# Kernel optimization log

Measured on AMD Instinct MI355X. Metric: run time of the kernel, lower is better.

## Reference

```python
import math
import jax, jax.numpy as jnp
import numpy as np

D_MODEL = 1024
N_HEADS = 16
D_HEAD = D_MODEL // N_HEADS


def get_alibi_slopes(n_heads: int) -> np.ndarray:
    def pow2_slopes(n):
        start = 2 ** (-2 ** (-(math.log2(n) - 3)))
        return np.array([start * start ** i for i in range(n)], dtype=np.float32)
    if math.log2(n_heads).is_integer():
        return pow2_slopes(n_heads)
    closest = 2 ** math.floor(math.log2(n_heads))
    slopes = pow2_slopes(closest)
    extra = pow2_slopes(2 * closest)[0::2][: n_heads - closest]
    return np.concatenate([slopes, extra], axis=0)


def setup_inputs() -> dict:
    key = jax.random.key(0)
    ks = jax.random.split(key, 9)
    B, S, D = 2, 2048, D_MODEL
    scale = 1.0 / math.sqrt(D)
    inp = {
        "x": jax.random.normal(ks[0], (B, S, D), dtype=jnp.float32),
        "Wq": jax.random.normal(ks[1], (D, D), dtype=jnp.float32) * scale,
        "bq": jnp.zeros((D,), dtype=jnp.float32),
        "Wk": jax.random.normal(ks[2], (D, D), dtype=jnp.float32) * scale,
        "bk": jnp.zeros((D,), dtype=jnp.float32),
        "Wv": jax.random.normal(ks[3], (D, D), dtype=jnp.float32) * scale,
        "bv": jnp.zeros((D,), dtype=jnp.float32),
        "Wo": jax.random.normal(ks[4], (D, D), dtype=jnp.float32) * scale,
        "bo": jnp.zeros((D,), dtype=jnp.float32),
    }
    return inp


def reference(x, Wq, bq, Wk, bk, Wv, bv, Wo, bo):
    B, S, D = x.shape
    H, Dh = N_HEADS, D_HEAD
    # projections (torch Linear: x @ W.T + b)
    q = (x @ Wq.T + bq).reshape(B, S, H, Dh).transpose(0, 2, 1, 3)  # [B,H,S,Dh]
    k = (x @ Wk.T + bk).reshape(B, S, H, Dh).transpose(0, 2, 1, 3)
    v = (x @ Wv.T + bv).reshape(B, S, H, Dh).transpose(0, 2, 1, 3)

    scores = jnp.einsum("bhqd,bhkd->bhqk", q, k) / math.sqrt(Dh)  # [B,H,S,S]

    slopes = jnp.asarray(get_alibi_slopes(H), dtype=scores.dtype)  # [H]
    pos = jnp.arange(S, dtype=scores.dtype)
    pos_diff = pos[None, :] - pos[:, None]                         # [S,S] (k - q)
    alibi = slopes[:, None, None] * pos_diff[None, :, :]           # [H,S,S]
    scores = scores + alibi[None]

    causal = jnp.tril(jnp.ones((S, S), dtype=bool))
    scores = jnp.where(causal[None, None], scores, -jnp.inf)

    weights = jax.nn.softmax(scores, axis=-1)
    y = jnp.einsum("bhqk,bhkd->bhqd", weights, v)                  # [B,H,S,Dh]
    y = y.transpose(0, 2, 1, 3).reshape(B, S, D)
    return y @ Wo.T + bo
```

## Files before the change

### kernel.cpp

```cpp
#include <hip/hip_runtime.h>

typedef unsigned short u16;
typedef unsigned int u32;
typedef short bf16x8 __attribute__((ext_vector_type(8)));
typedef float f32x4 __attribute__((ext_vector_type(4)));
typedef u16 u16x4 __attribute__((ext_vector_type(4)));

#define D_MODEL 1024
#define NHEADS 16
#define DHEAD 64
#define BATCH 2
#define SEQ 2048
#define NROWS (BATCH * SEQ)
#define NTILES (SEQ / 64)

static __device__ __forceinline__ u16 f2bf(float f) {
  u32 x = __float_as_uint(f);
  x += 0x7fffu + ((x >> 16) & 1u);
  return (u16)(x >> 16);
}

#define GLL16(gp, lp)                                             \
  __builtin_amdgcn_global_load_lds(                               \
      (const __attribute__((address_space(1))) u32*)(gp),         \
      (__attribute__((address_space(3))) u32*)(lp), 16, 0, 0)

__global__ __launch_bounds__(256) void castk(const float* __restrict__ in,
                                             u16* __restrict__ out, int n4) {
  int i = blockIdx.x * 256 + threadIdx.x;
  if (i >= n4) return;
  float4 v = ((const float4*)in)[i];
  u32 lo = (u32)f2bf(v.x) | ((u32)f2bf(v.y) << 16);
  u32 hi = (u32)f2bf(v.z) | ((u32)f2bf(v.w) << 16);
  ((uint2*)out)[i] = make_uint2(lo, hi);
}

__global__ __launch_bounds__(256) void castw(const float* __restrict__ w0,
                                             const float* __restrict__ w1,
                                             const float* __restrict__ w2,
                                             const float* __restrict__ w3,
                                             u16* __restrict__ o0,
                                             u16* __restrict__ o1,
                                             u16* __restrict__ o2,
                                             u16* __restrict__ o3) {
  const int z = blockIdx.z;
  const float* in = (z == 0) ? w0 : (z == 1) ? w1 : (z == 2) ? w2 : w3;
  u16* out = (z == 0) ? o0 : (z == 1) ? o1 : (z == 2) ? o2 : o3;
  int i = blockIdx.x * 256 + threadIdx.x;
  float4 v = ((const float4*)in)[i];
  u32 lo = (u32)f2bf(v.x) | ((u32)f2bf(v.y) << 16);
  u32 hi = (u32)f2bf(v.z) | ((u32)f2bf(v.w) << 16);
  ((uint2*)out)[i] = make_uint2(lo, hi);
}

template <int MODE>
__device__ __forceinline__ void gemm_core(const u16* __restrict__ A,
                                          const u16* __restrict__ Bw,
                                          const float* __restrict__ bias,
                                          u16* __restrict__ ob,
                                          float* __restrict__ of,
                                          int bm, int bn) {
  constexpr int K = 1024, N = 1024;
  __shared__ __attribute__((aligned(16))) u16 As[128 * 32];
  __shared__ __attribute__((aligned(16))) u16 Bs[128 * 32];
  const int tx = threadIdx.x;
  const int w = tx >> 6, lane = tx & 63;
  const int wm = w >> 1, wn = w & 1;
  const int c = lane & 15, g = lane >> 4;
  f32x4 acc[4][4];
  for (int m = 0; m < 4; ++m)
    for (int n = 0; n < 4; ++n) acc[m][n] = {0.f, 0.f, 0.f, 0.f};
  const int srow = w * 16 + (lane >> 2);
  const int sck = (lane & 3) * 8;
  for (int k0 = 0; k0 < K; k0 += 32) {
    for (int m = 0; m < 2; ++m) {
      GLL16(A + (size_t)(bm + m * 64 + srow) * K + k0 + sck,
            (char*)As + m * 4096 + w * 1024);
      GLL16(Bw + (size_t)(bn + m * 64 + srow) * K + k0 + sck,
            (char*)Bs + m * 4096 + w * 1024);
    }
    __syncthreads();
    bf16x8 af[4], bf_[4];
    for (int m = 0; m < 4; ++m)
      af[m] = *(const bf16x8*)(As + (wm * 64 + m * 16 + c) * 32 + g * 8);
    for (int n = 0; n < 4; ++n)
      bf_[n] = *(const bf16x8*)(Bs + (wn * 64 + n * 16 + c) * 32 + g * 8);
    for (int m = 0; m < 4; ++m)
      for (int n = 0; n < 4; ++n)
        acc[m][n] = __builtin_amdgcn_mfma_f32_16x16x32_bf16(af[m], bf_[n],
                                                            acc[m][n], 0, 0, 0);
    __syncthreads();
  }
  for (int n = 0; n < 4; ++n) {
    const int col = bn + wn * 64 + n * 16 + c;
    const float bv = bias[col];
    for (int m = 0; m < 4; ++m) {
      if (MODE == 2) {
        const int rs = bm + wm * 64 + m * 16 + g * 4;
        u16x4 pk;
        for (int r = 0; r < 4; ++r) pk[r] = f2bf(acc[m][n][r] + bv);
        const size_t vrow = (size_t)((rs >> 11) * NHEADS + (col >> 6)) * DHEAD +
                            (col & 63);
        *(u16x4*)(ob + vrow * SEQ + (rs & 2047)) = pk;
      } else {
        for (int r = 0; r < 4; ++r) {
          const int row = bm + wm * 64 + m * 16 + g * 4 + r;
          float v = acc[m][n][r] + bv;
          if (MODE == 1)
            of[(size_t)row * N + col] = v;
          else
            ob[(size_t)row * N + col] = f2bf(v);
        }
      }
    }
  }
}

__global__ __launch_bounds__(256) void gemm_qkv(const u16* __restrict__ xb,
                                                const u16* __restrict__ wq,
                                                const u16* __restrict__ wk,
                                                const float* __restrict__ bq,
                                                const float* __restrict__ bk,
                                                u16* __restrict__ q,
                                                u16* __restrict__ k) {
  const int z = blockIdx.z;
  const u16* W = (z == 0) ? wq : wk;
  const float* bi = (z == 0) ? bq : bk;
  u16* o = (z == 0) ? q : k;
  gemm_core<0>(xb, W, bi, o, nullptr, blockIdx.y * 128, blockIdx.x * 128);
}

__global__ __launch_bounds__(256) void gemm_v(const u16* __restrict__ xb,
                                              const u16* __restrict__ wv,
                                              const float* __restrict__ bv,
                                              u16* __restrict__ vt) {
  gemm_core<2>(xb, wv, bv, vt, nullptr, blockIdx.y * 128, blockIdx.x * 128);
}

__global__ __launch_bounds__(256) void gemm_o(const u16* __restrict__ yb,
                                              const u16* __restrict__ wo,
                                              const float* __restrict__ bo,
                                              float* __restrict__ out) {
  gemm_core<1>(yb, wo, bo, nullptr, out, blockIdx.y * 128, blockIdx.x * 128);
}

__global__ __launch_bounds__(256) void attn(const u16* __restrict__ qb,
                                            const u16* __restrict__ kb,
                                            const u16* __restrict__ vt,
                                            u16* __restrict__ yb) {
  __shared__ __attribute__((aligned(16))) u16 Qs[64 * 64];
  __shared__ __attribute__((aligned(16))) u16 Ks[2 * 64 * 64];
  __shared__ __attribute__((aligned(16))) u16 Vs[2 * 64 * 64];
  __shared__ __attribute__((aligned(16))) u16 Ps[4 * 16 * 64];
  const int tx = threadIdx.x;
  const int w = tx >> 6, lane = tx & 63;
  const int c = lane & 15, g = lane >> 4;
  const int bh = blockIdx.y;
  const int b = bh >> 4, h = bh & 15;
  const size_t rb = (size_t)b * SEQ;
  const size_t vtb = (size_t)bh * DHEAD;
  const float slope2 = exp2f(-0.5f * (float)(h + 1)) * 1.44269504f;
  const float S2 = 0.125f * 1.44269504f;

  const int strow = w * 8 + (lane >> 3);
  const int stck = lane & 7;

  for (int pass = 0; pass < 2; ++pass) {
    const int qi = pass ? (NTILES - 1 - blockIdx.x) : blockIdx.x;
    const int q0 = qi * 64;
    if (pass) __syncthreads();

    for (int m = 0; m < 2; ++m) {
      int row = m * 32 + strow;
      GLL16(qb + (rb + q0 + row) * D_MODEL + h * DHEAD +
                ((stck ^ (row & 7)) * 8),
            (char*)Qs + m * 4096 + w * 1024);
      GLL16(kb + (rb + row) * D_MODEL + h * DHEAD + ((stck ^ (row & 7)) * 8),
            (char*)Ks + m * 4096 + w * 1024);
      GLL16(vt + (vtb + row) * SEQ + ((stck ^ (row & 7)) * 8),
            (char*)Vs + m * 4096 + w * 1024);
    }

    float mrun[4], lsum[4];
    f32x4 acc[4];
    for (int r = 0; r < 4; ++r) { mrun[r] = -1e30f; lsum[r] = 0.f; }
    for (int d = 0; d < 4; ++d) acc[d] = {0.f, 0.f, 0.f, 0.f};
    const float qrow[4] = {(float)(q0 + w * 16 + g * 4 + 0),
                           (float)(q0 + w * 16 + g * 4 + 1),
                           (float)(q0 + w * 16 + g * 4 + 2),
                           (float)(q0 + w * 16 + g * 4 + 3)};
    const int qrowi = q0 + w * 16 + g * 4;

    int cur = 0;
    for (int kt = 0; kt <= qi; ++kt) {
      __syncthreads();
      if (kt < qi) {
        for (int m = 0; m < 2; ++m) {
          int row = m * 32 + strow;
          GLL16(kb + (rb + (kt + 1) * 64 + row) * D_MODEL + h * DHEAD +
                    ((stck ^ (row & 7)) * 8),
                (char*)Ks + (cur ^ 1) * 8192 + m * 4096 + w * 1024);
          GLL16(vt + (vtb + row) * SEQ + (kt + 1) * 64 +
                    ((stck ^ (row & 7)) * 8),
                (char*)Vs + (cur ^ 1) * 8192 + m * 4096 + w * 1024);
        }
      }

      bf16x8 aq[2];
      for (int ks = 0; ks < 2; ++ks)
        aq[ks] = *(const bf16x8*)((const char*)Qs + (w * 16 + c) * 128 +
                                  ((ks * 64 + g * 16) ^ ((c & 7) << 4)));
      f32x4 sc[4];
      for (int n = 0; n < 4; ++n) {
        sc[n] = {0.f, 0.f, 0.f, 0.f};
        for (int ks = 0; ks < 2; ++ks) {
          bf16x8 bk = *(const bf16x8*)((const char*)Ks + cur * 8192 +
                                       (n * 16 + c) * 128 +
                                       ((ks * 64 + g * 16) ^ ((c & 7) << 4)));
          sc[n] =
              __builtin_amdgcn_mfma_f32_16x16x32_bf16(aq[ks], bk, sc[n], 0, 0, 0);
        }
      }

      const int kbase = kt * 64 + c;
      const bool diag = (kt == qi);
      float p[4][4];
      for (int r = 0; r < 4; ++r) {
        const float base = slope2 * ((float)kbase - qrow[r]);
        float srow_[4];
        float rmax = -1e30f;
        for (int n = 0; n < 4; ++n) {
          float s = fmaf(sc[n][r], S2, base + slope2 * (float)(n * 16));
          if (diag && (kbase + n * 16 > qrowi + r)) s = -1e30f;
          srow_[n] = s;
          rmax = fmaxf(rmax, s);
        }
        for (int off = 1; off < 16; off <<= 1)
          rmax = fmaxf(rmax, __shfl_xor(rmax, off));
        const float mn = fmaxf(mrun[r], rmax);
        const float corr = exp2f(mrun[r] - mn);
        mrun[r] = mn;
        float rsum = 0.f;
        for (int n = 0; n < 4; ++n) {
          float pv = exp2f(srow_[n] - mn);
          p[n][r] = pv;
          rsum += pv;
        }
        for (int off = 1; off < 16; off <<= 1) rsum += __shfl_xor(rsum, off);
        lsum[r] = lsum[r] * corr + rsum;
        for (int d = 0; d < 4; ++d) acc[d][r] *= corr;
      }

      for (int n = 0; n < 4; ++n)
        for (int r = 0; r < 4; ++r) {
          const int row = g * 4 + r;
          *(u16*)((char*)Ps + w * 2048 + row * 128 +
                  (((n * 16 + c) * 2) ^ ((row & 7) << 4))) = f2bf(p[n][r]);
        }

      for (int ks = 0; ks < 2; ++ks) {
        bf16x8 pa = *(const bf16x8*)((const char*)Ps + w * 2048 + c * 128 +
                                     ((ks * 64 + g * 16) ^ ((c & 7) << 4)));
        for (int d = 0; d < 4; ++d) {
          bf16x8 vb_ = *(const bf16x8*)((const char*)Vs + cur * 8192 +
                                        (d * 16 + c) * 128 +
                                        ((ks * 64 + g * 16) ^ ((c & 7) << 4)));
          acc[d] = __builtin_amdgcn_mfma_f32_16x16x32_bf16(pa, vb_, acc[d], 0, 0, 0);
        }
      }
      cur ^= 1;
    }

    for (int d = 0; d < 4; ++d)
      for (int r = 0; r < 4; ++r) {
        const int qlocal = w * 16 + g * 4 + r;
        float o = acc[d][r] / lsum[r];
        yb[(rb + q0 + qlocal) * D_MODEL + h * DHEAD + d * 16 + c] = f2bf(o);
      }
  }
}

extern "C" void kernel_launch(void* const* d_in, const int* in_sizes, int n_in,
                              void* d_out, int out_size, void* d_ws,
                              size_t ws_size, hipStream_t stream) {
  const float* x = (const float*)d_in[0];
  const float* Wq = (const float*)d_in[1];
  const float* bq = (const float*)d_in[2];
  const float* Wk = (const float*)d_in[3];
  const float* bk = (const float*)d_in[4];
  const float* Wv = (const float*)d_in[5];
  const float* bv = (const float*)d_in[6];
  const float* Wo = (const float*)d_in[7];
  const float* bo = (const float*)d_in[8];
  float* out = (float*)d_out;

  char* ws = (char*)d_ws;
  u16* xb = (u16*)(ws + (size_t)0);
  u16* wqb = (u16*)(ws + ((size_t)8 << 20));
  u16* wkb = (u16*)(ws + ((size_t)10 << 20));
  u16* wvb = (u16*)(ws + ((size_t)12 << 20));
  u16* wob = (u16*)(ws + ((size_t)14 << 20));
  u16* qb = (u16*)(ws + ((size_t)16 << 20));
  u16* kb = (u16*)(ws + ((size_t)24 << 20));
  u16* vtb = (u16*)(ws + ((size_t)32 << 20));
  u16* yb = xb;

  castk<<<4096, 256, 0, stream>>>(x, xb, NROWS * D_MODEL / 4);
  castw<<<dim3(1024, 1, 4), 256, 0, stream>>>(Wq, Wk, Wv, Wo, wqb, wkb, wvb,
                                              wob);

  gemm_qkv<<<dim3(8, 32, 2), 256, 0, stream>>>(xb, wqb, wkb, bq, bk, qb, kb);
  gemm_v<<<dim3(8, 32, 1), 256, 0, stream>>>(xb, wvb, bv, vtb);
  attn<<<dim3(NTILES / 2, 32, 1), 256, 0, stream>>>(qb, kb, vtb, yb);
  gemm_o<<<dim3(8, 32, 1), 256, 0, stream>>>(yb, wob, bo, out);
}
```

Measured before the change: 245.8 us.

## Double-buffer GEMM K-tiles, reschedule attention grid, compute row sums via MFMA

```diff
diff --git a/kernel.cpp b/kernel.cpp
--- a/kernel.cpp
+++ b/kernel.cpp
@@ -61,8 +61,8 @@
                                           float* __restrict__ of,
                                           int bm, int bn) {
   constexpr int K = 1024, N = 1024;
-  __shared__ __attribute__((aligned(16))) u16 As[128 * 32];
-  __shared__ __attribute__((aligned(16))) u16 Bs[128 * 32];
+  __shared__ __attribute__((aligned(16))) u16 As[2][128 * 32];
+  __shared__ __attribute__((aligned(16))) u16 Bs[2][128 * 32];
   const int tx = threadIdx.x;
   const int w = tx >> 6, lane = tx & 63;
   const int wm = w >> 1, wn = w & 1;
@@ -72,24 +72,33 @@
     for (int n = 0; n < 4; ++n) acc[m][n] = {0.f, 0.f, 0.f, 0.f};
   const int srow = w * 16 + (lane >> 2);
   const int sck = (lane & 3) * 8;
+  for (int m = 0; m < 2; ++m) {
+    GLL16(A + (size_t)(bm + m * 64 + srow) * K + sck,
+          (char*)As[0] + m * 4096 + w * 1024);
+    GLL16(Bw + (size_t)(bn + m * 64 + srow) * K + sck,
+          (char*)Bs[0] + m * 4096 + w * 1024);
+  }
+  int cur = 0;
   for (int k0 = 0; k0 < K; k0 += 32) {
-    for (int m = 0; m < 2; ++m) {
-      GLL16(A + (size_t)(bm + m * 64 + srow) * K + k0 + sck,
-            (char*)As + m * 4096 + w * 1024);
-      GLL16(Bw + (size_t)(bn + m * 64 + srow) * K + k0 + sck,
-            (char*)Bs + m * 4096 + w * 1024);
-    }
     __syncthreads();
+    if (k0 + 32 < K) {
+      for (int m = 0; m < 2; ++m) {
+        GLL16(A + (size_t)(bm + m * 64 + srow) * K + k0 + 32 + sck,
+              (char*)As[cur ^ 1] + m * 4096 + w * 1024);
+        GLL16(Bw + (size_t)(bn + m * 64 + srow) * K + k0 + 32 + sck,
+              (char*)Bs[cur ^ 1] + m * 4096 + w * 1024);
+      }
+    }
     bf16x8 af[4], bf_[4];
     for (int m = 0; m < 4; ++m)
-      af[m] = *(const bf16x8*)(As + (wm * 64 + m * 16 + c) * 32 + g * 8);
+      af[m] = *(const bf16x8*)(As[cur] + (wm * 64 + m * 16 + c) * 32 + g * 8);
     for (int n = 0; n < 4; ++n)
-      bf_[n] = *(const bf16x8*)(Bs + (wn * 64 + n * 16 + c) * 32 + g * 8);
+      bf_[n] = *(const bf16x8*)(Bs[cur] + (wn * 64 + n * 16 + c) * 32 + g * 8);
     for (int m = 0; m < 4; ++m)
       for (int n = 0; n < 4; ++n)
         acc[m][n] = __builtin_amdgcn_mfma_f32_16x16x32_bf16(af[m], bf_[n],
                                                             acc[m][n], 0, 0, 0);
-    __syncthreads();
+    cur ^= 1;
   }
   for (int n = 0; n < 4; ++n) {
     const int col = bn + wn * 64 + n * 16 + c;
@@ -149,14 +158,17 @@
                                             const u16* __restrict__ vt,
                                             u16* __restrict__ yb) {
   __shared__ __attribute__((aligned(16))) u16 Qs[64 * 64];
-  __shared__ __attribute__((aligned(16))) u16 Ks[2 * 64 * 64];
-  __shared__ __attribute__((aligned(16))) u16 Vs[2 * 64 * 64];
+  __shared__ __attribute__((aligned(16))) u16 Ks[2][64 * 64];
+  __shared__ __attribute__((aligned(16))) u16 Vs[2][64 * 64];
   __shared__ __attribute__((aligned(16))) u16 Ps[4 * 16 * 64];
   const int tx = threadIdx.x;
   const int w = tx >> 6, lane = tx & 63;
   const int c = lane & 15, g = lane >> 4;
-  const int bh = blockIdx.y;
+  const int f = blockIdx.x;
+  const int bh = (f & 7) * 4 + ((f >> 3) & 3);
+  const int qi = NTILES - 1 - (f >> 5);
   const int b = bh >> 4, h = bh & 15;
+  const int q0 = qi * 64;
   const size_t rb = (size_t)b * SEQ;
   const size_t vtb = (size_t)bh * DHEAD;
   const float slope2 = exp2f(-0.5f * (float)(h + 1)) * 1.44269504f;
@@ -165,119 +177,108 @@
   const int strow = w * 8 + (lane >> 3);
   const int stck = lane & 7;
 
-  for (int pass = 0; pass < 2; ++pass) {
-    const int qi = pass ? (NTILES - 1 - blockIdx.x) : blockIdx.x;
-    const int q0 = qi * 64;
-    if (pass) __syncthreads();
-
-    for (int m = 0; m < 2; ++m) {
-      int row = m * 32 + strow;
-      GLL16(qb + (rb + q0 + row) * D_MODEL + h * DHEAD +
-                ((stck ^ (row & 7)) * 8),
-            (char*)Qs + m * 4096 + w * 1024);
-      GLL16(kb + (rb + row) * D_MODEL + h * DHEAD + ((stck ^ (row & 7)) * 8),
-            (char*)Ks + m * 4096 + w * 1024);
-      GLL16(vt + (vtb + row) * SEQ + ((stck ^ (row & 7)) * 8),
-            (char*)Vs + m * 4096 + w * 1024);
-    }
-
-    float mrun[4], lsum[4];
-    f32x4 acc[4];
-    for (int r = 0; r < 4; ++r) { mrun[r] = -1e30f; lsum[r] = 0.f; }
-    for (int d = 0; d < 4; ++d) acc[d] = {0.f, 0.f, 0.f, 0.f};
-    const float qrow[4] = {(float)(q0 + w * 16 + g * 4 + 0),
-                           (float)(q0 + w * 16 + g * 4 + 1),
-                           (float)(q0 + w * 16 + g * 4 + 2),
-                           (float)(q0 + w * 16 + g * 4 + 3)};
-    const int qrowi = q0 + w * 16 + g * 4;
-
-    int cur = 0;
-    for (int kt = 0; kt <= qi; ++kt) {
-      __syncthreads();
-      if (kt < qi) {
-        for (int m = 0; m < 2; ++m) {
-          int row = m * 32 + strow;
-          GLL16(kb + (rb + (kt + 1) * 64 + row) * D_MODEL + h * DHEAD +
-                    ((stck ^ (row & 7)) * 8),
-                (char*)Ks + (cur ^ 1) * 8192 + m * 4096 + w * 1024);
-          GLL16(vt + (vtb + row) * SEQ + (kt + 1) * 64 +
-                    ((stck ^ (row & 7)) * 8),
-                (char*)Vs + (cur ^ 1) * 8192 + m * 4096 + w * 1024);
-        }
-      }
-
-      bf16x8 aq[2];
-      for (int ks = 0; ks < 2; ++ks)
-        aq[ks] = *(const bf16x8*)((const char*)Qs + (w * 16 + c) * 128 +
-                                  ((ks * 64 + g * 16) ^ ((c & 7) << 4)));
-      f32x4 sc[4];
+  for (int m = 0; m < 2; ++m) {
+    int row = m * 32 + strow;
+    GLL16(qb + (rb + q0 + row) * D_MODEL + h * DHEAD + ((stck ^ (row & 7)) * 8),
+          (char*)Qs + m * 4096 + w * 1024);
+    GLL16(kb + (rb + row) * D_MODEL + h * DHEAD + ((stck ^ (row & 7)) * 8),
+          (char*)Ks[0] + m * 4096 + w * 1024);
+    GLL16(vt + (vtb + row) * SEQ + ((stck ^ (row & 7)) * 8),
+          (char*)Vs[0] + m * 4096 + w * 1024);
+  }
+
+  float mrun[4];
+  f32x4 acc[4], lacc;
+  for (int r = 0; r < 4; ++r) mrun[r] = -1e30f;
+  for (int d = 0; d < 4; ++d) acc[d] = {0.f, 0.f, 0.f, 0.f};
+  lacc = {0.f, 0.f, 0.f, 0.f};
+  bf16x8 ones;
+  for (int j = 0; j < 8; ++j) ones[j] = (short)0x3F80;
+  const float qrow[4] = {(float)(q0 + w * 16 + g * 4 + 0),
+                         (float)(q0 + w * 16 + g * 4 + 1),
+                         (float)(q0 + w * 16 + g * 4 + 2),
+                         (float)(q0 + w * 16 + g * 4 + 3)};
+  const int qrowi = q0 + w * 16 + g * 4;
+
+  int cur = 0;
+  for (int kt = 0; kt <= qi; ++kt) {
+    __syncthreads();
+    if (kt < qi) {
+      for (int m = 0; m < 2; ++m) {
+        int row = m * 32 + strow;
+        GLL16(kb + (rb + (kt + 1) * 64 + row) * D_MODEL + h * DHEAD +
+                  ((stck ^ (row & 7)) * 8),
+              (char*)Ks[cur ^ 1] + m * 4096 + w * 1024);
+        GLL16(vt + (vtb + row) * SEQ + (kt + 1) * 64 +
+                  ((stck ^ (row & 7)) * 8),
+              (char*)Vs[cur ^ 1] + m * 4096 + w * 1024);
+      }
+    }
+
+    bf16x8 aq[2];
+    for (int ks = 0; ks < 2; ++ks)
+      aq[ks] = *(const bf16x8*)((const char*)Qs + (w * 16 + c) * 128 +
+                                ((ks * 64 + g * 16) ^ ((c & 7) << 4)));
+    f32x4 sc[4];
+    for (int n = 0; n < 4; ++n) {
+      sc[n] = {0.f, 0.f, 0.f, 0.f};
+      for (int ks = 0; ks < 2; ++ks) {
+        bf16x8 bk = *(const bf16x8*)((const char*)Ks[cur] + (n * 16 + c) * 128 +
+                                     ((ks * 64 + g * 16) ^ ((c & 7) << 4)));
+        sc[n] = __builtin_amdgcn_mfma_f32_16x16x32_bf16(aq[ks], bk, sc[n], 0, 0, 0);
+      }
+    }
+
+    const int kbase = kt * 64 + c;
+    const bool diag = (kt == qi);
+    float p[4][4];
+    for (int r = 0; r < 4; ++r) {
+      const float base = slope2 * ((float)kbase - qrow[r]);
+      float srow_[4];
+      float rmax = -1e30f;
       for (int n = 0; n < 4; ++n) {
-        sc[n] = {0.f, 0.f, 0.f, 0.f};
-        for (int ks = 0; ks < 2; ++ks) {
-          bf16x8 bk = *(const bf16x8*)((const char*)Ks + cur * 8192 +
-                                       (n * 16 + c) * 128 +
-                                       ((ks * 64 + g * 16) ^ ((c & 7) << 4)));
-          sc[n] =
-              __builtin_amdgcn_mfma_f32_16x16x32_bf16(aq[ks], bk, sc[n], 0, 0, 0);
-        }
-      }
-
-      const int kbase = kt * 64 + c;
-      const bool diag = (kt == qi);
-      float p[4][4];
+        float s = fmaf(sc[n][r], S2, base + slope2 * (float)(n * 16));
+        if (diag && (kbase + n * 16 > qrowi + r)) s = -1e30f;
+        srow_[n] = s;
+        rmax = fmaxf(rmax, s);
+      }
+      for (int off = 1; off < 16; off <<= 1)
+        rmax = fmaxf(rmax, __shfl_xor(rmax, off));
+      const float mn = fmaxf(mrun[r], rmax);
+      const float corr = exp2f(mrun[r] - mn);
+      mrun[r] = mn;
+      for (int n = 0; n < 4; ++n) p[n][r] = exp2f(srow_[n] - mn);
+      lacc[r] *= corr;
+      for (int d = 0; d < 4; ++d) acc[d][r] *= corr;
+    }
+
+    for (int n = 0; n < 4; ++n)
       for (int r = 0; r < 4; ++r) {
-        const float base = slope2 * ((float)kbase - qrow[r]);
-        float srow_[4];
-        float rmax = -1e30f;
-        for (int n = 0; n < 4; ++n) {
-          float s = fmaf(sc[n][r], S2, base + slope2 * (float)(n * 16));
-          if (diag && (kbase + n * 16 > qrowi + r)) s = -1e30f;
-          srow_[n] = s;
-          rmax = fmaxf(rmax, s);
-        }
-        for (int off = 1; off < 16; off <<= 1)
-          rmax = fmaxf(rmax, __shfl_xor(rmax, off));
-        const float mn = fmaxf(mrun[r], rmax);
-        const float corr = exp2f(mrun[r] - mn);
-        mrun[r] = mn;
-        float rsum = 0.f;
-        for (int n = 0; n < 4; ++n) {
-          float pv = exp2f(srow_[n] - mn);
-          p[n][r] = pv;
-          rsum += pv;
-        }
-        for (int off = 1; off < 16; off <<= 1) rsum += __shfl_xor(rsum, off);
-        lsum[r] = lsum[r] * corr + rsum;
-        for (int d = 0; d < 4; ++d) acc[d][r] *= corr;
-      }
-
-      for (int n = 0; n < 4; ++n)
-        for (int r = 0; r < 4; ++r) {
-          const int row = g * 4 + r;
-          *(u16*)((char*)Ps + w * 2048 + row * 128 +
-                  (((n * 16 + c) * 2) ^ ((row & 7) << 4))) = f2bf(p[n][r]);
-        }
-
-      for (int ks = 0; ks < 2; ++ks) {
-        bf16x8 pa = *(const bf16x8*)((const char*)Ps + w * 2048 + c * 128 +
-                                     ((ks * 64 + g * 16) ^ ((c & 7) << 4)));
-        for (int d = 0; d < 4; ++d) {
-          bf16x8 vb_ = *(const bf16x8*)((const char*)Vs + cur * 8192 +
-                                        (d * 16 + c) * 128 +
-                                        ((ks * 64 + g * 16) ^ ((c & 7) << 4)));
-          acc[d] = __builtin_amdgcn_mfma_f32_16x16x32_bf16(pa, vb_, acc[d], 0, 0, 0);
-        }
-      }
-      cur ^= 1;
-    }
-
-    for (int d = 0; d < 4; ++d)
-      for (int r = 0; r < 4; ++r) {
-        const int qlocal = w * 16 + g * 4 + r;
-        float o = acc[d][r] / lsum[r];
-        yb[(rb + q0 + qlocal) * D_MODEL + h * DHEAD + d * 16 + c] = f2bf(o);
-      }
-  }
+        const int row = g * 4 + r;
+        *(u16*)((char*)Ps + w * 2048 + row * 128 +
+                (((n * 16 + c) * 2) ^ ((row & 7) << 4))) = f2bf(p[n][r]);
+      }
+
+    for (int ks = 0; ks < 2; ++ks) {
+      bf16x8 pa = *(const bf16x8*)((const char*)Ps + w * 2048 + c * 128 +
+                                   ((ks * 64 + g * 16) ^ ((c & 7) << 4)));
+      for (int d = 0; d < 4; ++d) {
+        bf16x8 vb_ = *(const bf16x8*)((const char*)Vs[cur] +
+                                      (d * 16 + c) * 128 +
+                                      ((ks * 64 + g * 16) ^ ((c & 7) << 4)));
+        acc[d] = __builtin_amdgcn_mfma_f32_16x16x32_bf16(pa, vb_, acc[d], 0, 0, 0);
+      }
+      lacc = __builtin_amdgcn_mfma_f32_16x16x32_bf16(pa, ones, lacc, 0, 0, 0);
+    }
+    cur ^= 1;
+  }
+
+  for (int d = 0; d < 4; ++d)
+    for (int r = 0; r < 4; ++r) {
+      const int qlocal = w * 16 + g * 4 + r;
+      float o = acc[d][r] / lacc[r];
+      yb[(rb + q0 + qlocal) * D_MODEL + h * DHEAD + d * 16 + c] = f2bf(o);
+    }
 }
 
 extern "C" void kernel_launch(void* const* d_in, const int* in_sizes, int n_in,
@@ -311,6 +312,6 @@
 
   gemm_qkv<<<dim3(8, 32, 2), 256, 0, stream>>>(xb, wqb, wkb, bq, bk, qb, kb);
   gemm_v<<<dim3(8, 32, 1), 256, 0, stream>>>(xb, wvb, bv, vtb);
-  attn<<<dim3(NTILES / 2, 32, 1), 256, 0, stream>>>(qb, kb, vtb, yb);
+  attn<<<dim3(NTILES * NHEADS * BATCH, 1, 1), 256, 0, stream>>>(qb, kb, vtb, yb);
   gemm_o<<<dim3(8, 32, 1), 256, 0, stream>>>(yb, wob, bo, out);
 }
```

After: 228.1 us. 7.2% less time.
